# Kernel optimization log

Measured on AMD Instinct MI355X. Metric: run time of the kernel, lower is better.

Reference implementation:

```python
import jax, jax.numpy as jnp
import numpy as np

SIGMA2_MU = 0.5  # hyper_params['sigma2_mu']
R = 128          # number of spatial basis functions
NV = 2000        # number of query points
KM1 = 30         # K - 1


def setup_inputs() -> dict:
    key = jax.random.key(0)
    k1, k2, k3, k4 = jax.random.split(key, 4)
    Xi_evals = jax.random.normal(k1, (R, NV), dtype=jnp.float32)
    vec_W_post_mean = jax.random.normal(k2, (R * KM1, 1), dtype=jnp.float32)
    vec_W_post_cov = jax.random.normal(k3, (R * KM1, R * KM1), dtype=jnp.float32)
    C_mu = jax.random.normal(k4, (NV, 1), dtype=jnp.float32)
    return {"Xi_evals": Xi_evals, "vec_W_post_mean": vec_W_post_mean,
            "vec_W_post_cov": vec_W_post_cov, "C_mu": C_mu}


def reference(Xi_evals, vec_W_post_mean, vec_W_post_cov, C_mu):
    # Xi_evals: (r, Nv); vec_W_post_mean: (r*(K-1), 1); vec_W_post_cov: (r*(K-1), r*(K-1))
    r, Nv = Xi_evals.shape
    Km1 = vec_W_post_mean.shape[0] // r
    K = Km1 + 1
    X = Xi_evals.T                                # (Nv, r)
    # kron(x^T, I_{K-1}) @ w  ==  X @ W  with W = w.reshape(r, K-1)
    W = vec_W_post_mean.reshape(r, Km1)
    Post_mean_c = X @ W                           # (Nv, K-1)
    # kron(x^T, I) @ Cov @ kron(x, I): quadratic form over r-blocks
    C4 = vec_W_post_cov.reshape(r, Km1, r, Km1)   # (i, k, j, l)
    A = jnp.einsum('vi,ikjl->vkjl', X, C4)        # (Nv, K-1, r, K-1)
    Post_cov_c = jnp.einsum('vkjl,vj->vkl', A, X) # (Nv, K-1, K-1)
    Post_mean_coefs = jnp.concatenate([C_mu, Post_mean_c], axis=1)  # (Nv, K)
    Post_cov_mats = jnp.zeros((Nv, K, K), dtype=Xi_evals.dtype)
    Post_cov_mats = Post_cov_mats.at[:, 0, 0].set(SIGMA2_MU)
    Post_cov_mats = Post_cov_mats.at[:, 1:, 1:].set(Post_cov_c)
    return Post_mean_coefs, Post_cov_mats
```

## Files before the change

kernel.cpp:

```cpp
#include <hip/hip_runtime.h>

typedef _Float16 f16;
typedef _Float16 f16x8 __attribute__((ext_vector_type(8)));
typedef float    f32x16 __attribute__((ext_vector_type(16)));

#define NV      2000
#define RR      128
#define KM1     30
#define KKOUT   31
#define NQ      900
#define QQ      961
#define COV_OFF 62000

#define B5_BYTES 17104896
#define XH_BYTES 524288

#define PERM_BLKS  3840
#define XC1_BLKS   128
#define ZERO_BLKS  1877
#define MEAN_BLKS  248
#define PREP_GRID  (PERM_BLKS + XC1_BLKS + ZERO_BLKS + MEAN_BLKS)

__global__ void prep_kernel(const float* __restrict__ Xi,
                            const float* __restrict__ Wm,
                            const float* __restrict__ cov,
                            const float* __restrict__ Cmu,
                            f16* __restrict__ B5,
                            f16* __restrict__ Xh,
                            float* __restrict__ outm,
                            float* __restrict__ oc) {
    __shared__ float rowS[3840];
    int b = blockIdx.x, tid = threadIdx.x;
    if (b < PERM_BLKS) {
        int i = b / 30, k = b - i * 30;
        int g = i >> 4;
        int j0 = g << 4;
        int W = 128 - j0;
        int lo = (i - j0) * 30;
        const float* src = cov + (size_t)b * 3840 + j0 * 30;
        for (int t = tid; t < W * 30; t += 256)
            rowS[t] = (t >= lo) ? src[t] : 0.f;
        __syncthreads();
        int n2 = (127 - i) * 15;
        for (int idx = tid; idx < n2; idx += 256) {
            int j = i + 1 + idx / 15;
            int p = idx - (j - i - 1) * 15;
            const float2 v2 = *(const float2*)(cov + (size_t)(j * 30 + k) * 3840 + i * 30 + 2 * p);
            rowS[(j - j0) * 30 + 2 * p]     += v2.x;
            rowS[(j - j0) * 30 + 2 * p + 1] += v2.y;
        }
        __syncthreads();
        int t_st = i & 15;
        int nOct = W >> 3;
        for (int it = tid; it < nOct * 30; it += 256) {
            int oct = it / 30, l = it - oct * 30;
            int j = j0 + oct * 8;
            int s = j >> 4, kq = (j >> 3) & 1;
            int q = k * 30 + l, qt = q >> 5, l31 = q & 31;
            int kz, slot;
            if (g < 4) { kz = g;     slot = s - g; }
            else       { kz = 7 - g; slot = s + 1; }
            f16 vals[8];
#pragma unroll
            for (int d = 0; d < 8; ++d) vals[d] = (f16)rowS[(j + d - j0) * 30 + l];
            f16* dst = B5 + ((((size_t)(qt * 4 + kz) * 16 + t_st) * 9 + slot) << 9)
                          + (kq * 32 + l31) * 8;
            *(uint4*)dst = *(uint4*)vals;
        }
        return;
    }
    b -= PERM_BLKS;
    if (b < XC1_BLKS) {
        int t = b * 256 + tid;
        int v = t & 2047, rc = t >> 11;
        f16 vals[8];
#pragma unroll
        for (int d = 0; d < 8; ++d) {
            float x = (v < NV) ? Xi[(rc * 8 + d) * NV + v] : 0.f;
            vals[d] = (f16)x;
        }
        *(uint4*)(Xh + (size_t)v * 128 + rc * 8) = *(uint4*)vals;
        return;
    }
    b -= XC1_BLKS;
    if (b < ZERO_BLKS) {
        size_t idx = ((size_t)b * 256 + tid) * 4;
        if (idx < (size_t)NV * QQ) {
            unsigned rem = (unsigned)(idx % QQ);
            float4 zv;
            zv.x = (rem == 0u)   ? 0.5f : 0.f;
            zv.y = (rem == 960u) ? 0.5f : 0.f;
            zv.z = (rem == 959u) ? 0.5f : 0.f;
            zv.w = (rem == 958u) ? 0.5f : 0.f;
            *(float4*)(oc + idx) = zv;
        }
        return;
    }
    b -= ZERO_BLKS;
    int t2 = b * 256 + tid;
    int c = t2 >> 11, v = t2 & 2047;
    if (v >= NV || c >= KKOUT) return;
    if (c == 0) { outm[(size_t)v * KKOUT] = Cmu[v]; return; }
    float acc = 0.f;
    const float* w = Wm + (c - 1);
#pragma unroll 8
    for (int i = 0; i < RR; ++i)
        acc = fmaf(Xi[i * NV + v], w[i * KM1], acc);
    outm[(size_t)v * KKOUT + c] = acc;
}

__device__ __forceinline__ void load9(f16x8 (&b)[9], const f16* p) {
#pragma unroll
    for (int m = 0; m < 9; ++m)
        b[m] = *(const f16x8*)(p + m * 512);
}

template<int KZ, int T>
__device__ __forceinline__ void stage_compute(int l31,
                                              const f16x8 (&bv)[9],
                                              const f16x8 (&xj)[2][8],
                                              f32x16 (&acc)[2]) {
    constexpr int NA = 8 - KZ, NB = 1 + KZ;
    const int srcl = l31 + ((T >> 3) << 5);
    f16 xA[2], xB[2];
#pragma unroll
    for (int fm = 0; fm < 2; ++fm) {
        unsigned short ha = __builtin_bit_cast(unsigned short, (f16)xj[fm][KZ][T & 7]);
        unsigned short hb = __builtin_bit_cast(unsigned short, (f16)xj[fm][7 - KZ][T & 7]);
        int pa = __shfl((int)ha, srcl, 64);
        int pb = __shfl((int)hb, srcl, 64);
        xA[fm] = __builtin_bit_cast(f16, (unsigned short)pa);
        xB[fm] = __builtin_bit_cast(f16, (unsigned short)pb);
    }
#pragma unroll
    for (int m = 0; m < NA; ++m)
#pragma unroll
        for (int fm = 0; fm < 2; ++fm)
            acc[fm] = __builtin_amdgcn_mfma_f32_32x32x16_f16(xj[fm][KZ + m] * xA[fm], bv[m], acc[fm], 0, 0, 0);
#pragma unroll
    for (int m2 = 0; m2 < NB; ++m2)
#pragma unroll
        for (int fm = 0; fm < 2; ++fm)
            acc[fm] = __builtin_amdgcn_mfma_f32_32x32x16_f16(xj[fm][7 - KZ + m2] * xB[fm], bv[NA + m2], acc[fm], 0, 0, 0);
}

template<int KZH, int ST>
struct Stage {
    static __device__ __forceinline__ void run(const f16* gs, f16x8 (&buf)[3][9],
                                               const f16x8 (&xj)[2][8],
                                               f32x16 (&acc)[2], int l31) {
        if constexpr (ST + 2 < 32)
            load9(buf[(ST + 2) % 3], gs + (size_t)(ST + 2) * 4608);
        stage_compute<KZH * 2 + (ST >> 4), ST & 15>(l31, buf[ST % 3], xj, acc);
        Stage<KZH, ST + 1>::run(gs, buf, xj, acc, l31);
    }
};
template<int KZH>
struct Stage<KZH, 32> {
    static __device__ __forceinline__ void run(const f16*, f16x8 (&)[3][9],
                                               const f16x8 (&)[2][8],
                                               f32x16 (&)[2], int) {}
};

__launch_bounds__(256, 2)
__global__ void gemm7_kernel(const f16* __restrict__ B5,
                             const f16* __restrict__ Xh,
                             float* __restrict__ out_cov) {
    const int bid = blockIdx.x;
    const int p = (bid & 7) * 58 + (bid >> 3);
    const int qt = p >> 4;
    const int r  = p & 15;
    const int y = r >> 1, h = r & 1;
    const int tid = threadIdx.x, lane = tid & 63, w = tid >> 6;
    const int l31 = lane & 31, kq = lane >> 5;
    const int v0 = y * 256 + w * 64;
    const int vr = v0 + l31;

    f16x8 xj[2][8];
#pragma unroll
    for (int fm = 0; fm < 2; ++fm)
#pragma unroll
        for (int u = 0; u < 8; ++u)
            xj[fm][u] = *(const f16x8*)(Xh + (size_t)(vr + fm * 32) * 128 + u * 16 + kq * 8);

    const f16* gbase = B5 + ((size_t)qt * 64 + (size_t)h * 32) * 4608 + lane * 8;

    f16x8 buf[3][9];
    load9(buf[0], gbase);
    load9(buf[1], gbase + 4608);

    f32x16 acc[2] = {};
    if (h == 0) Stage<0, 0>::run(gbase, buf, xj, acc, l31);
    else        Stage<1, 0>::run(gbase, buf, xj, acc, l31);

    const int q = qt * 32 + l31;
    if (q >= NQ) return;
    const int kk = q / 30, ll = q - kk * 30;
    float* cb = out_cov + (kk + 1) * KKOUT + (ll + 1);
#pragma unroll
    for (int fm = 0; fm < 2; ++fm) {
        int vb = v0 + fm * 32 + 4 * kq;
#pragma unroll
        for (int rr = 0; rr < 16; ++rr) {
            int v = vb + (rr & 3) + 8 * (rr >> 2);
            if (v < NV) atomicAdd(cb + (size_t)v * QQ, acc[fm][rr]);
        }
    }
}

extern "C" void kernel_launch(void* const* d_in, const int* in_sizes, int n_in,
                              void* d_out, int out_size, void* d_ws, size_t ws_size,
                              hipStream_t stream) {
    const float* Xi  = (const float*)d_in[0];
    const float* Wm  = (const float*)d_in[1];
    const float* Cov = (const float*)d_in[2];
    const float* Cmu = (const float*)d_in[3];
    float* out      = (float*)d_out;
    float* out_mean = out;
    float* out_cov  = out + COV_OFF;
    f16* B5 = (f16*)d_ws;
    f16* Xh = (f16*)((char*)d_ws + B5_BYTES);

    prep_kernel <<<PREP_GRID, 256, 0, stream>>>(Xi, Wm, Cov, Cmu, B5, Xh,
                                                out_mean, out_cov);
    gemm7_kernel<<<464, 256, 0, stream>>>(B5, Xh, out_cov);
}
```

Baseline: 161.9 us.

## Stage B tiles through LDS with async global_load_lds triple buffering

Before this change each of the four waves loaded the full 9-fragment B tile per stage from global memory into registers, so every block fetched the same data four times. Now each wave copies a quarter of the tile into a shared LDS triple buffer using async global-to-LDS loads. Stages are synchronised with explicit vmcnt waits and barriers, and every wave then reads the whole tile from LDS. This cuts redundant global traffic and register pressure from the register triple buffer, at the cost of a barrier per stage and extra LDS reads.

```diff
diff --git a/kernel.cpp b/kernel.cpp
--- a/kernel.cpp
+++ b/kernel.cpp
@@ -109,18 +109,32 @@
     outm[(size_t)v * KKOUT + c] = acc;
 }
 
-__device__ __forceinline__ void load9(f16x8 (&b)[9], const f16* p) {
-#pragma unroll
-    for (int m = 0; m < 9; ++m)
-        b[m] = *(const f16x8*)(p + m * 512);
+__device__ __forceinline__ void stage_issue(const f16* gs, f16* ls, int w, int lane) {
+    const f16* g = gs + w * 1152;
+    f16* l = ls + w * 1152;
+    __builtin_amdgcn_global_load_lds(
+        (const __attribute__((address_space(1))) unsigned int*)(const void*)(g + lane * 8),
+        (__attribute__((address_space(3))) unsigned int*)(void*)(l),
+        16, 0, 0);
+    __builtin_amdgcn_global_load_lds(
+        (const __attribute__((address_space(1))) unsigned int*)(const void*)(g + 512 + lane * 8),
+        (__attribute__((address_space(3))) unsigned int*)(void*)(l + 512),
+        16, 0, 0);
+    __builtin_amdgcn_global_load_lds(
+        (const __attribute__((address_space(1))) unsigned int*)(const void*)(g + 1024 + lane * 2),
+        (__attribute__((address_space(3))) unsigned int*)(void*)(l + 1024),
+        4, 0, 0);
 }
 
 template<int KZ, int T>
-__device__ __forceinline__ void stage_compute(int l31,
-                                              const f16x8 (&bv)[9],
+__device__ __forceinline__ void stage_compute(int l31, const f16* lb,
                                               const f16x8 (&xj)[2][8],
                                               f32x16 (&acc)[2]) {
     constexpr int NA = 8 - KZ, NB = 1 + KZ;
+    f16x8 bv[9];
+#pragma unroll
+    for (int m = 0; m < 9; ++m)
+        bv[m] = *(const f16x8*)(lb + m * 512);
     const int srcl = l31 + ((T >> 3) << 5);
     f16 xA[2], xB[2];
 #pragma unroll
@@ -146,26 +160,33 @@
 
 template<int KZH, int ST>
 struct Stage {
-    static __device__ __forceinline__ void run(const f16* gs, f16x8 (&buf)[3][9],
+    static __device__ __forceinline__ void run(const f16* gs, f16* lbuf,
+                                               const f16* lrd,
                                                const f16x8 (&xj)[2][8],
-                                               f32x16 (&acc)[2], int l31) {
+                                               f32x16 (&acc)[2],
+                                               int l31, int w, int lane) {
+        if constexpr (ST == 31)
+            asm volatile("s_waitcnt vmcnt(0) lgkmcnt(0)\ns_barrier" ::: "memory");
+        else
+            asm volatile("s_waitcnt vmcnt(3) lgkmcnt(0)\ns_barrier" ::: "memory");
         if constexpr (ST + 2 < 32)
-            load9(buf[(ST + 2) % 3], gs + (size_t)(ST + 2) * 4608);
-        stage_compute<KZH * 2 + (ST >> 4), ST & 15>(l31, buf[ST % 3], xj, acc);
-        Stage<KZH, ST + 1>::run(gs, buf, xj, acc, l31);
+            stage_issue(gs + (size_t)(ST + 2) * 4608, lbuf + ((ST + 2) % 3) * 4608, w, lane);
+        stage_compute<KZH * 2 + (ST >> 4), ST & 15>(l31, lrd + (ST % 3) * 4608, xj, acc);
+        Stage<KZH, ST + 1>::run(gs, lbuf, lrd, xj, acc, l31, w, lane);
     }
 };
 template<int KZH>
 struct Stage<KZH, 32> {
-    static __device__ __forceinline__ void run(const f16*, f16x8 (&)[3][9],
+    static __device__ __forceinline__ void run(const f16*, f16*, const f16*,
                                                const f16x8 (&)[2][8],
-                                               f32x16 (&)[2], int) {}
+                                               f32x16 (&)[2], int, int, int) {}
 };
 
 __launch_bounds__(256, 2)
-__global__ void gemm7_kernel(const f16* __restrict__ B5,
+__global__ void gemm9_kernel(const f16* __restrict__ B5,
                              const f16* __restrict__ Xh,
                              float* __restrict__ out_cov) {
+    __shared__ f16 lbuf[3 * 4608];
     const int bid = blockIdx.x;
     const int p = (bid & 7) * 58 + (bid >> 3);
     const int qt = p >> 4;
@@ -183,15 +204,15 @@
         for (int u = 0; u < 8; ++u)
             xj[fm][u] = *(const f16x8*)(Xh + (size_t)(vr + fm * 32) * 128 + u * 16 + kq * 8);
 
-    const f16* gbase = B5 + ((size_t)qt * 64 + (size_t)h * 32) * 4608 + lane * 8;
-
-    f16x8 buf[3][9];
-    load9(buf[0], gbase);
-    load9(buf[1], gbase + 4608);
+    const f16* gstage = B5 + ((size_t)qt * 64 + (size_t)h * 32) * 4608;
+    const f16* lrd = lbuf + lane * 8;
+
+    stage_issue(gstage,        lbuf,        w, lane);
+    stage_issue(gstage + 4608, lbuf + 4608, w, lane);
 
     f32x16 acc[2] = {};
-    if (h == 0) Stage<0, 0>::run(gbase, buf, xj, acc, l31);
-    else        Stage<1, 0>::run(gbase, buf, xj, acc, l31);
+    if (h == 0) Stage<0, 0>::run(gstage, lbuf, lrd, xj, acc, l31, w, lane);
+    else        Stage<1, 0>::run(gstage, lbuf, lrd, xj, acc, l31, w, lane);
 
     const int q = qt * 32 + l31;
     if (q >= NQ) return;
@@ -223,5 +244,5 @@
 
     prep_kernel <<<PREP_GRID, 256, 0, stream>>>(Xi, Wm, Cov, Cmu, B5, Xh,
                                                 out_mean, out_cov);
-    gemm7_kernel<<<464, 256, 0, stream>>>(B5, Xh, out_cov);
-}
+    gemm9_kernel<<<464, 256, 0, stream>>>(B5, Xh, out_cov);
+}
```

Result: faster. 156.8 us (-3.1%).
